# Kernel optimization log

Hardware: AMD Instinct MI355X
Metric: run time of the kernel (lower is better)

Reference implementation:

```python
import jax, jax.numpy as jnp
import numpy as np

N, E, IN, H, L, NB, G = 50000, 300000, 64, 256, 4, 181, 64
EPS = 1e-5
NEG_SLOPE = 0.2


def segment_softmax(e, seg, n):
    m = jax.ops.segment_max(e, seg, num_segments=n)
    a = jnp.exp(e - m[seg])
    d = jax.ops.segment_sum(a, seg, num_segments=n)
    return a / d[seg]


def setup_inputs() -> dict:
    key = jax.random.key(0)
    ks = jax.random.split(key, 32)
    p = lambda k, shape, fan: (jax.random.normal(k, shape, jnp.float32) / np.sqrt(fan)).astype(jnp.float32)
    inp = {}
    inp["x"] = jax.random.normal(ks[0], (N, IN), jnp.float32)
    inp["edge_index"] = jax.random.randint(ks[1], (2, E), 0, N, jnp.int64)
    inp["batch"] = jnp.sort(jax.random.randint(ks[2], (N,), 0, G, jnp.int64))
    inp["W_in"] = p(ks[3], (H, IN), IN); inp["b_in"] = jnp.zeros((H,), jnp.float32)
    inp["Wl"] = p(ks[4], (L, H, H), H); inp["bl"] = jnp.zeros((L, H), jnp.float32)
    inp["Wr"] = p(ks[5], (L, H, H), H); inp["br"] = jnp.zeros((L, H), jnp.float32)
    inp["att"] = p(ks[6], (L, H), H)
    inp["bias_c"] = jnp.zeros((L, H), jnp.float32)
    inp["ln_g"] = jnp.ones((L, H), jnp.float32); inp["ln_b"] = jnp.zeros((L, H), jnp.float32)
    inp["Wg1"] = p(ks[7], (H, H), H); inp["bg1"] = jnp.zeros((H,), jnp.float32)
    inp["Wg2"] = p(ks[8], (1, H), H); inp["bg2"] = jnp.zeros((1,), jnp.float32)
    inp["Ws"] = p(ks[9], (H, H), H); inp["bs"] = jnp.zeros((H,), jnp.float32)
    inp["Wc"] = p(ks[10], (NB, H), H); inp["bc"] = jnp.zeros((NB,), jnp.float32)
    inp["Wr1"] = p(ks[11], (128, H), H); inp["br1"] = jnp.zeros((128,), jnp.float32)
    inp["Wr2"] = p(ks[12], (1, 128), 128); inp["br2"] = jnp.zeros((1,), jnp.float32)
    return inp


def reference(x, edge_index, batch, W_in, b_in, Wl, bl, Wr, br, att, bias_c, ln_g, ln_b,
              Wg1, bg1, Wg2, bg2, Ws, bs, Wc, bc, Wr1, br1, Wr2, br2):
    n = x.shape[0]
    x = x @ W_in.T + b_in  # input projection -> [N,H]
    loops = jnp.arange(n)
    src = jnp.concatenate([edge_index[0], loops])  # GATv2 add_self_loops=True
    dst = jnp.concatenate([edge_index[1], loops])
    for l in range(L):
        x_res = x
        xl = x @ Wl[l].T + bl[l]  # lin_l (source)
        xr = x @ Wr[l].T + br[l]  # lin_r (target)
        h = jax.nn.leaky_relu(xl[src] + xr[dst], NEG_SLOPE)  # [E+N, H]
        e = h @ att[l]                                       # [E+N]
        alpha = segment_softmax(e, dst, n)
        out = jax.ops.segment_sum(alpha[:, None] * xl[src], dst, num_segments=n) + bias_c[l]
        mu = out.mean(-1, keepdims=True)
        var = out.var(-1, keepdims=True)
        out = (out - mu) / jnp.sqrt(var + EPS) * ln_g[l] + ln_b[l]
        x = jax.nn.relu(out) + x_res  # dropout is identity at eval
    gate = jax.nn.relu(x @ Wg1.T + bg1) @ Wg2.T + bg2  # [N,1]
    a = segment_softmax(gate[:, 0], batch, G)
    pooled = jax.ops.segment_sum(a[:, None] * x, batch, num_segments=G)  # [G,H]
    z = jax.nn.relu(pooled @ Ws.T + bs)
    cls_logits = z @ Wc.T + bc                                   # [G,NB]
    residual = jnp.tanh(jax.nn.relu(z @ Wr1.T + br1) @ Wr2.T + br2)[:, 0]  # [G]
    return cls_logits, residual
```

## Files before the change

### kernel.cpp

```cpp
#include <hip/hip_runtime.h>
#include <math.h>

#define N_NODES 50000
#define N_EDGES 300000
#define IN_DIM 64
#define H 256
#define LAYERS 4
#define NB 181
#define NGRAPH 64
#define EE (N_EDGES + N_NODES)
#define NEG_SLOPE 0.2f
#define LN_EPS 1e-5f

typedef unsigned short u16;
typedef __attribute__((ext_vector_type(8))) short short8;
typedef __attribute__((ext_vector_type(4))) float floatx4;

__device__ __forceinline__ u16 f2b(float f) {
  unsigned int u = __builtin_bit_cast(unsigned int, f);
  unsigned int r = (u + 0x7FFFu + ((u >> 16) & 1u)) >> 16;
  return (u16)r;
}
__device__ __forceinline__ float b2f(u16 b) {
  return __builtin_bit_cast(float, ((unsigned int)b) << 16);
}

__device__ __forceinline__ float wave_reduce_sum(float v) {
  #pragma unroll
  for (int off = 32; off > 0; off >>= 1) v += __shfl_xor(v, off, 64);
  return v;
}

__global__ void cast_bf16_kernel(const float* __restrict__ in, u16* __restrict__ out, int n4) {
  int i = blockIdx.x * 256 + threadIdx.x;
  if (i < n4) {
    float4 f = ((const float4*)in)[i];
    ushort4 o;
    o.x = f2b(f.x); o.y = f2b(f.y); o.z = f2b(f.z); o.w = f2b(f.w);
    ((ushort4*)out)[i] = o;
  }
}

__global__ void cast_weights_kernel(
    const float* __restrict__ W_in, const float* __restrict__ Wg1,
    const float* __restrict__ Wl, const float* __restrict__ Wr,
    u16* __restrict__ win_bf, u16* __restrict__ wg1_bf,
    u16* __restrict__ wl_bf, u16* __restrict__ wr_bf)
{
  int i = blockIdx.x * 256 + threadIdx.x;
  int which = blockIdx.y;
  const float* s; u16* dd; int n4;
  if (which == 0)      { s = W_in; dd = win_bf; n4 = H * IN_DIM / 4; }
  else if (which == 1) { s = Wg1;  dd = wg1_bf; n4 = H * H / 4; }
  else if (which == 2) { s = Wl;   dd = wl_bf;  n4 = LAYERS * H * H / 4; }
  else                 { s = Wr;   dd = wr_bf;  n4 = LAYERS * H * H / 4; }
  if (i < n4) {
    float4 f = ((const float4*)s)[i];
    ushort4 o;
    o.x = f2b(f.x); o.y = f2b(f.y); o.z = f2b(f.z); o.w = f2b(f.w);
    ((ushort4*)dd)[i] = o;
  }
}

__global__ void init_counts_kernel(int* __restrict__ cnt) {
  int i = blockIdx.x * 256 + threadIdx.x;
  if (i < N_NODES) cnt[i] = 1;
}

__global__ void count_edges_kernel(const int* __restrict__ dst, int* __restrict__ cnt) {
  int e = blockIdx.x * 256 + threadIdx.x;
  if (e < N_EDGES) atomicAdd(&cnt[dst[e]], 1);
}

__global__ void scan_blocks_kernel(const int* __restrict__ cnt, int* __restrict__ partial,
                                   int* __restrict__ bsums, int n) {
  __shared__ int buf[256];
  int tid = threadIdx.x;
  int i = blockIdx.x * 256 + tid;
  buf[tid] = (i < n) ? cnt[i] : 0;
  __syncthreads();
  #pragma unroll
  for (int off = 1; off < 256; off <<= 1) {
    int t = (tid >= off) ? buf[tid - off] : 0;
    __syncthreads();
    buf[tid] += t;
    __syncthreads();
  }
  if (i < n) partial[i] = buf[tid];
  if (tid == 255) bsums[blockIdx.x] = buf[255];
}

__global__ void scan_sums_kernel(int* __restrict__ bsums, int nblk) {
  __shared__ int buf[256];
  int tid = threadIdx.x;
  buf[tid] = (tid < nblk) ? bsums[tid] : 0;
  __syncthreads();
  #pragma unroll
  for (int off = 1; off < 256; off <<= 1) {
    int t = (tid >= off) ? buf[tid - off] : 0;
    __syncthreads();
    buf[tid] += t;
    __syncthreads();
  }
  if (tid < nblk) bsums[tid] = buf[tid];
}

__global__ void scan_write_kernel(const int* __restrict__ partial, const int* __restrict__ bsums,
                                  int* __restrict__ rowp, int n) {
  int i = blockIdx.x * 256 + threadIdx.x;
  if (i < n) {
    int b = blockIdx.x;
    int off = (b > 0) ? bsums[b - 1] : 0;
    rowp[i + 1] = partial[i] + off;
    if (i == 0) rowp[0] = 0;
  }
}

__global__ void fill_self_kernel(const int* __restrict__ rowp, int* __restrict__ col,
                                 int* __restrict__ fillpos) {
  int i = blockIdx.x * 256 + threadIdx.x;
  if (i < N_NODES) {
    int p = rowp[i];
    col[p] = i;
    fillpos[i] = p + 1;
  }
}

__global__ void fill_edges_kernel(const int* __restrict__ src, const int* __restrict__ dst,
                                  int* __restrict__ fillpos, int* __restrict__ col) {
  int e = blockIdx.x * 256 + threadIdx.x;
  if (e < N_EDGES) {
    int d = dst[e];
    int p = atomicAdd(&fillpos[d], 1);
    col[p] = src[e];
  }
}

#define GTM 128
#define GTK 64
#define LDB 72
#define SSTR 132

__global__ __launch_bounds__(256) void gemm_proj_kernel(
    const u16* __restrict__ A, const u16* __restrict__ W,
    const float* __restrict__ bias, u16* __restrict__ outbf, int M, int K)
{
  __shared__ u16 smem[2 * GTM * LDB];
  u16* As = smem;
  u16* Bs = smem + GTM * LDB;
  int tid = threadIdx.x;
  int lane = tid & 63;
  int wave = tid >> 6;
  int wm = (wave >> 1) * 64;
  int wn = (wave & 1) * 64;
  int bm = blockIdx.y * GTM;
  int n0 = blockIdx.x * 128;
  int lr = tid >> 3;
  int lc = (tid & 7) * 8;

  floatx4 zero4 = {0.f, 0.f, 0.f, 0.f};
  floatx4 acc[4][4];
  #pragma unroll
  for (int i = 0; i < 4; i++)
    #pragma unroll
    for (int j = 0; j < 4; j++) acc[i][j] = zero4;

  int q8 = (lane >> 4) * 8;
  int mrow = lane & 15;

  for (int k0 = 0; k0 < K; k0 += GTK) {
    __syncthreads();
    #pragma unroll
    for (int p = 0; p < 4; p++) {
      int row = lr + p * 32;
      int gr = bm + row;
      short8 av = {0, 0, 0, 0, 0, 0, 0, 0};
      if (gr < M) av = *(const short8*)&A[(size_t)gr * K + k0 + lc];
      *(short8*)&As[row * LDB + lc] = av;
      short8 bv = *(const short8*)&W[(size_t)(n0 + row) * K + k0 + lc];
      *(short8*)&Bs[row * LDB + lc] = bv;
    }
    __syncthreads();
    #pragma unroll
    for (int h = 0; h < 2; h++) {
      short8 af[4], bf[4];
      #pragma unroll
      for (int i = 0; i < 4; i++)
        af[i] = *(const short8*)&As[(wm + i * 16 + mrow) * LDB + h * 32 + q8];
      #pragma unroll
      for (int j = 0; j < 4; j++)
        bf[j] = *(const short8*)&Bs[(wn + j * 16 + mrow) * LDB + h * 32 + q8];
      #pragma unroll
      for (int i = 0; i < 4; i++)
        #pragma unroll
        for (int j = 0; j < 4; j++)
          acc[i][j] = __builtin_amdgcn_mfma_f32_16x16x32_bf16(af[i], bf[j], acc[i][j], 0, 0, 0);
    }
  }

  __syncthreads();
  u16* stage = smem;
  int ccol = lane & 15;
  int crow4 = (lane >> 4) * 4;
  #pragma unroll
  for (int j = 0; j < 4; j++) {
    float bv = bias[n0 + wn + j * 16 + ccol];
    #pragma unroll
    for (int i = 0; i < 4; i++) {
      #pragma unroll
      for (int r = 0; r < 4; r++) {
        int row = wm + i * 16 + crow4 + r;
        stage[row * SSTR + wn + j * 16 + ccol] = f2b(acc[i][j][r] + bv);
      }
    }
  }
  __syncthreads();
  int rr = tid >> 1;
  int c0 = (tid & 1) * 64;
  int grow = bm + rr;
  if (grow < M) {
    const ushort4* sp = (const ushort4*)&stage[rr * SSTR + c0];
    ushort4* gp = (ushort4*)&outbf[(size_t)grow * H + n0 + c0];
    #pragma unroll
    for (int q = 0; q < 16; q++) gp[q] = sp[q];
  }
}

#define DTM 64
#define AST 264
#define SSTR2 132

__global__ __launch_bounds__(256) void gemm_dual2_kernel(
    const u16* __restrict__ A, const u16* __restrict__ Wlb, const u16* __restrict__ Wrb,
    const float* __restrict__ biasL, const float* __restrict__ biasR,
    u16* __restrict__ outL, u16* __restrict__ outR, int M)
{
  __shared__ u16 As[DTM * AST];
  __shared__ u16 Bs[128 * LDB];
  int tid = threadIdx.x;
  int lane = tid & 63;
  int wave = tid >> 6;
  int wn = wave * 32;
  int bm = blockIdx.x * DTM;
  int mrow = lane & 15;
  int q8 = (lane >> 4) * 8;
  int ccol = lane & 15;
  int crow4 = (lane >> 4) * 4;

  {
    int col = (tid & 31) * 8;
    int r0 = tid >> 5;
    #pragma unroll
    for (int it = 0; it < 8; it++) {
      int row = r0 + it * 8;
      int gr = bm + row;
      short8 av = {0, 0, 0, 0, 0, 0, 0, 0};
      if (gr < M) av = *(const short8*)&A[(size_t)gr * H + col];
      *(short8*)&As[row * AST + col] = av;
    }
  }

  floatx4 zero4 = {0.f, 0.f, 0.f, 0.f};

  for (int nt = 0; nt < 4; nt++) {
    const u16* W = (nt < 2) ? Wlb : Wrb;
    const float* bias = (nt < 2) ? biasL : biasR;
    u16* outp = (nt < 2) ? outL : outR;
    int n0 = (nt & 1) * 128;

    floatx4 acc[4][2];
    #pragma unroll
    for (int i = 0; i < 4; i++) {
      acc[i][0] = zero4;
      acc[i][1] = zero4;
    }

    for (int k0 = 0; k0 < H; k0 += 64) {
      __syncthreads();
      {
        int col = (tid & 7) * 8;
        int r0 = tid >> 3;
        #pragma unroll
        for (int p2 = 0; p2 < 4; p2++) {
          int row = r0 + p2 * 32;
          short8 bv = *(const short8*)&W[(size_t)(n0 + row) * H + k0 + col];
          *(short8*)&Bs[row * LDB + col] = bv;
        }
      }
      __syncthreads();
      #pragma unroll
      for (int h = 0; h < 2; h++) {
        short8 af[4], bf[2];
        #pragma unroll
        for (int i = 0; i < 4; i++)
          af[i] = *(const short8*)&As[(i * 16 + mrow) * AST + k0 + h * 32 + q8];
        #pragma unroll
        for (int j = 0; j < 2; j++)
          bf[j] = *(const short8*)&Bs[(wn + j * 16 + mrow) * LDB + h * 32 + q8];
        #pragma unroll
        for (int i = 0; i < 4; i++)
          #pragma unroll
          for (int j = 0; j < 2; j++)
            acc[i][j] = __builtin_amdgcn_mfma_f32_16x16x32_bf16(af[i], bf[j], acc[i][j], 0, 0, 0);
      }
    }

    __syncthreads();
    u16* stage = Bs;
    #pragma unroll
    for (int j = 0; j < 2; j++) {
      float bv = bias[n0 + wn + j * 16 + ccol];
      #pragma unroll
      for (int i = 0; i < 4; i++) {
        #pragma unroll
        for (int r = 0; r < 4; r++) {
          int row = i * 16 + crow4 + r;
          stage[row * SSTR2 + wn + j * 16 + ccol] = f2b(acc[i][j][r] + bv);
        }
      }
    }
    __syncthreads();
    {
      int row = tid >> 2;
      int c0 = (tid & 3) * 32;
      int grow = bm + row;
      if (grow < M) {
        #pragma unroll
        for (int q = 0; q < 8; q++)
          *(ushort4*)&outp[(size_t)grow * H + n0 + c0 + q * 4] =
              *(const ushort4*)&stage[row * SSTR2 + c0 + q * 4];
      }
    }
  }
}

__global__ __launch_bounds__(256) void gemm_gate_kernel(
    const u16* __restrict__ A, const u16* __restrict__ W,
    const float* __restrict__ bias, const float* __restrict__ Wg2,
    float* __restrict__ gate, int M)
{
  __shared__ u16 smem[2 * GTM * LDB];
  u16* As = smem;
  u16* Bs = smem + GTM * LDB;
  int tid = threadIdx.x;
  int lane = tid & 63;
  int wave = tid >> 6;
  int wm = (wave >> 1) * 64;
  int wn = (wave & 1) * 64;
  int bm = blockIdx.y * GTM;
  int bn = blockIdx.x * 128;
  int lr = tid >> 3;
  int lc = (tid & 7) * 8;

  floatx4 zero4 = {0.f, 0.f, 0.f, 0.f};
  floatx4 acc[4][4];
  #pragma unroll
  for (int i = 0; i < 4; i++)
    #pragma unroll
    for (int j = 0; j < 4; j++) acc[i][j] = zero4;

  int q8 = (lane >> 4) * 8;
  int mrow = lane & 15;

  for (int k0 = 0; k0 < H; k0 += GTK) {
    __syncthreads();
    #pragma unroll
    for (int p = 0; p < 4; p++) {
      int row = lr + p * 32;
      int gr = bm + row;
      short8 av = {0, 0, 0, 0, 0, 0, 0, 0};
      if (gr < M) av = *(const short8*)&A[(size_t)gr * H + k0 + lc];
      *(short8*)&As[row * LDB + lc] = av;
      short8 bv = *(const short8*)&W[(size_t)(bn + row) * H + k0 + lc];
      *(short8*)&Bs[row * LDB + lc] = bv;
    }
    __syncthreads();
    #pragma unroll
    for (int h = 0; h < 2; h++) {
      short8 af[4], bf[4];
      #pragma unroll
      for (int i = 0; i < 4; i++)
        af[i] = *(const short8*)&As[(wm + i * 16 + mrow) * LDB + h * 32 + q8];
      #pragma unroll
      for (int j = 0; j < 4; j++)
        bf[j] = *(const short8*)&Bs[(wn + j * 16 + mrow) * LDB + h * 32 + q8];
      #pragma unroll
      for (int i = 0; i < 4; i++)
        #pragma unroll
        for (int j = 0; j < 4; j++)
          acc[i][j] = __builtin_amdgcn_mfma_f32_16x16x32_bf16(af[i], bf[j], acc[i][j], 0, 0, 0);
    }
  }

  int ccol = lane & 15;
  float bv[4], wv[4];
  #pragma unroll
  for (int j = 0; j < 4; j++) {
    int col = bn + wn + j * 16 + ccol;
    bv[j] = bias[col];
    wv[j] = Wg2[col];
  }
  #pragma unroll
  for (int i = 0; i < 4; i++) {
    #pragma unroll
    for (int r = 0; r < 4; r++) {
      float p = 0.f;
      #pragma unroll
      for (int j = 0; j < 4; j++) {
        float hcol = fmaxf(acc[i][j][r] + bv[j], 0.f);
        p += hcol * wv[j];
      }
      p += __shfl_xor(p, 1, 64);
      p += __shfl_xor(p, 2, 64);
      p += __shfl_xor(p, 4, 64);
      p += __shfl_xor(p, 8, 64);
      int row = bm + wm + i * 16 + (lane >> 4) * 4 + r;
      if ((lane & 15) == 0 && row < M) atomicAdd(&gate[row], p);
    }
  }
}

__global__ __launch_bounds__(256) void layer_fused_kernel(
    const u16* __restrict__ xl, const u16* __restrict__ xr,
    u16* __restrict__ xbf,
    const int* __restrict__ rowp, const int* __restrict__ col,
    const float* __restrict__ att, const float* __restrict__ bias_c,
    const float* __restrict__ ln_g, const float* __restrict__ ln_b)
{
  int lane = threadIdx.x & 63;
  int v = blockIdx.x * 4 + (threadIdx.x >> 6);
  if (v >= N_NODES) return;
  int f4 = lane << 2;
  size_t rowbase = (size_t)v * H;
  ushort4 xr4 = *(const ushort4*)&xr[rowbase + f4];
  float xrx = b2f(xr4.x), xry = b2f(xr4.y), xrz = b2f(xr4.z), xrw = b2f(xr4.w);
  float4 attv = *(const float4*)&att[f4];
  int beg = rowp[v], end = rowp[v + 1];
  float m = -INFINITY, d = 0.f;
  float ox = 0.f, oy = 0.f, oz = 0.f, ow = 0.f;
  int p = beg;
  for (; p + 2 <= end; p += 2) {
    int u0 = col[p];
    int u1 = col[p + 1];
    ushort4 a04 = *(const ushort4*)&xl[(size_t)u0 * H + f4];
    ushort4 a14 = *(const ushort4*)&xl[(size_t)u1 * H + f4];
    float a0x = b2f(a04.x), a0y = b2f(a04.y), a0z = b2f(a04.z), a0w = b2f(a04.w);
    float a1x = b2f(a14.x), a1y = b2f(a14.y), a1z = b2f(a14.z), a1w = b2f(a14.w);
    float t0x = a0x + xrx; t0x = t0x > 0.f ? t0x : NEG_SLOPE * t0x;
    float t0y = a0y + xry; t0y = t0y > 0.f ? t0y : NEG_SLOPE * t0y;
    float t0z = a0z + xrz; t0z = t0z > 0.f ? t0z : NEG_SLOPE * t0z;
    float t0w = a0w + xrw; t0w = t0w > 0.f ? t0w : NEG_SLOPE * t0w;
    float t1x = a1x + xrx; t1x = t1x > 0.f ? t1x : NEG_SLOPE * t1x;
    float t1y = a1y + xry; t1y = t1y > 0.f ? t1y : NEG_SLOPE * t1y;
    float t1z = a1z + xrz; t1z = t1z > 0.f ? t1z : NEG_SLOPE * t1z;
    float t1w = a1w + xrw; t1w = t1w > 0.f ? t1w : NEG_SLOPE * t1w;
    float pe0 = t0x * attv.x + t0y * attv.y + t0z * attv.z + t0w * attv.w;
    float pe1 = t1x * attv.x + t1y * attv.y + t1z * attv.z + t1w * attv.w;
    #pragma unroll
    for (int off = 32; off > 0; off >>= 1) {
      pe0 += __shfl_xor(pe0, off, 64);
      pe1 += __shfl_xor(pe1, off, 64);
    }
    float mn = fmaxf(m, fmaxf(pe0, pe1));
    float sc = __expf(m - mn);
    float w0 = __expf(pe0 - mn);
    float w1 = __expf(pe1 - mn);
    d = fmaf(d, sc, w0 + w1);
    ox = fmaf(ox, sc, fmaf(w0, a0x, w1 * a1x));
    oy = fmaf(oy, sc, fmaf(w0, a0y, w1 * a1y));
    oz = fmaf(oz, sc, fmaf(w0, a0z, w1 * a1z));
    ow = fmaf(ow, sc, fmaf(w0, a0w, w1 * a1w));
    m = mn;
  }
  if (p < end) {
    int u0 = col[p];
    ushort4 a04 = *(const ushort4*)&xl[(size_t)u0 * H + f4];
    float a0x = b2f(a04.x), a0y = b2f(a04.y), a0z = b2f(a04.z), a0w = b2f(a04.w);
    float t0x = a0x + xrx; t0x = t0x > 0.f ? t0x : NEG_SLOPE * t0x;
    float t0y = a0y + xry; t0y = t0y > 0.f ? t0y : NEG_SLOPE * t0y;
    float t0z = a0z + xrz; t0z = t0z > 0.f ? t0z : NEG_SLOPE * t0z;
    float t0w = a0w + xrw; t0w = t0w > 0.f ? t0w : NEG_SLOPE * t0w;
    float pe0 = t0x * attv.x + t0y * attv.y + t0z * attv.z + t0w * attv.w;
    pe0 = wave_reduce_sum(pe0);
    float mn = fmaxf(m, pe0);
    float sc = __expf(m - mn);
    float w0 = __expf(pe0 - mn);
    d = fmaf(d, sc, w0);
    ox = fmaf(ox, sc, w0 * a0x);
    oy = fmaf(oy, sc, w0 * a0y);
    oz = fmaf(oz, sc, w0 * a0z);
    ow = fmaf(ow, sc, w0 * a0w);
    m = mn;
  }
  float invd = 1.0f / d;
  float4 bc4 = *(const float4*)&bias_c[f4];
  ox = ox * invd + bc4.x;
  oy = oy * invd + bc4.y;
  oz = oz * invd + bc4.z;
  ow = ow * invd + bc4.w;
  float s = wave_reduce_sum(ox + oy + oz + ow);
  float mean = s * (1.0f / H);
  float cx = ox - mean, cy = oy - mean, cz = oz - mean, cw = ow - mean;
  float sq = wave_reduce_sum(cx * cx + cy * cy + cz * cz + cw * cw);
  float rstd = rsqrtf(sq * (1.0f / H) + LN_EPS);
  float4 g4 = *(const float4*)&ln_g[f4];
  float4 b4 = *(const float4*)&ln_b[f4];
  ushort4 xres4 = *(const ushort4*)&xbf[rowbase + f4];
  float yx = fmaxf(cx * rstd * g4.x + b4.x, 0.f) + b2f(xres4.x);
  float yy = fmaxf(cy * rstd * g4.y + b4.y, 0.f) + b2f(xres4.y);
  float yz = fmaxf(cz * rstd * g4.z + b4.z, 0.f) + b2f(xres4.z);
  float yw = fmaxf(cw * rstd * g4.w + b4.w, 0.f) + b2f(xres4.w);
  ushort4 yb;
  yb.x = f2b(yx); yb.y = f2b(yy); yb.z = f2b(yz); yb.w = f2b(yw);
  *(ushort4*)&xbf[rowbase + f4] = yb;
}

__global__ void gate_init_kernel(float* __restrict__ gate, const float* __restrict__ bg2,
                                 int* __restrict__ gstart, int* __restrict__ gend) {
  int i = blockIdx.x * 256 + threadIdx.x;
  if (i < N_NODES) gate[i] = bg2[0];
  if (i < NGRAPH) { gstart[i] = 0; gend[i] = 0; }
}

__global__ void gbounds_kernel(const int* __restrict__ batch, int* __restrict__ gstart,
                               int* __restrict__ gend) {
  int i = blockIdx.x * 256 + threadIdx.x;
  if (i < N_NODES) {
    int b = batch[i];
    if (i == 0 || batch[i - 1] != b) gstart[b] = i;
    if (i == N_NODES - 1 || batch[i + 1] != b) gend[b] = i + 1;
  }
}

__global__ __launch_bounds__(256) void pool_prep_kernel(
    const float* __restrict__ gate, const int* __restrict__ gstart,
    const int* __restrict__ gend, float* __restrict__ gmax, float* __restrict__ gdinv,
    float* __restrict__ pooled)
{
  __shared__ float red[256];
  int g = blockIdx.x, tid = threadIdx.x;
  pooled[(size_t)g * H + tid] = 0.f;
  int s = gstart[g], e = gend[g];
  float lm = -INFINITY;
  for (int i = s + tid; i < e; i += 256) lm = fmaxf(lm, gate[i]);
  red[tid] = lm;
  __syncthreads();
  for (int off = 128; off; off >>= 1) {
    if (tid < off) red[tid] = fmaxf(red[tid], red[tid + off]);
    __syncthreads();
  }
  float m = red[0];
  __syncthreads();
  float lsum = 0.0f;
  for (int i = s + tid; i < e; i += 256) lsum += __expf(gate[i] - m);
  red[tid] = lsum;
  __syncthreads();
  for (int off = 128; off; off >>= 1) {
    if (tid < off) red[tid] += red[tid + off];
    __syncthreads();
  }
  if (tid == 0) {
    gmax[g] = m;
    gdinv[g] = (s < e) ? 1.0f / red[0] : 0.0f;
  }
}

__global__ __launch_bounds__(256) void pool_accum_kernel(
    const float* __restrict__ gate, const u16* __restrict__ xbf,
    const int* __restrict__ batch, const float* __restrict__ gmax,
    const float* __restrict__ gdinv, float* __restrict__ pooled)
{
  __shared__ float wl[128];
  __shared__ int gl[128];
  int b0 = blockIdx.x * 128;
  int tid = threadIdx.x;
  if (tid < 128) {
    int v = b0 + tid;
    if (v < N_NODES) {
      int g = batch[v];
      gl[tid] = g;
      wl[tid] = __expf(gate[v] - gmax[g]) * gdinv[g];
    } else {
      gl[tid] = -1;
      wl[tid] = 0.f;
    }
  }
  __syncthreads();
  int cnt = min(128, N_NODES - b0);
  float acc = 0.f;
  int cur = gl[0];
  for (int j = 0; j < cnt; j++) {
    int g = gl[j];
    if (g != cur) {
      atomicAdd(&pooled[(size_t)cur * H + tid], acc);
      acc = 0.f;
      cur = g;
    }
    acc += wl[j] * b2f(xbf[(size_t)(b0 + j) * H + tid]);
  }
  if (cur >= 0) atomicAdd(&pooled[(size_t)cur * H + tid], acc);
}

__global__ __launch_bounds__(256) void head_kernel(
    const float* __restrict__ pooled,
    const float* __restrict__ Ws, const float* __restrict__ bs,
    const float* __restrict__ Wc, const float* __restrict__ bc,
    const float* __restrict__ Wr1, const float* __restrict__ br1,
    const float* __restrict__ Wr2, const float* __restrict__ br2,
    float* __restrict__ out)
{
  __shared__ float psh[256];
  __shared__ float zsh[256];
  __shared__ float r1sh[128];
  int g = blockIdx.x, tid = threadIdx.x;
  psh[tid] = pooled[(size_t)g * H + tid];
  __syncthreads();
  {
    float acc = bs[tid];
    const float4* wr = (const float4*)&Ws[(size_t)tid * H];
    for (int k4 = 0; k4 < H / 4; k4++) {
      float4 wv = wr[k4];
      float4 av = *(const float4*)&psh[k4 * 4];
      acc += av.x * wv.x + av.y * wv.y + av.z * wv.z + av.w * wv.w;
    }
    zsh[tid] = fmaxf(acc, 0.f);
  }
  __syncthreads();
  if (tid < NB) {
    float acc = bc[tid];
    const float4* wr = (const float4*)&Wc[(size_t)tid * H];
    for (int k4 = 0; k4 < H / 4; k4++) {
      float4 wv = wr[k4];
      float4 av = *(const float4*)&zsh[k4 * 4];
      acc += av.x * wv.x + av.y * wv.y + av.z * wv.z + av.w * wv.w;
    }
    out[(size_t)g * NB + tid] = acc;
  }
  if (tid < 128) {
    float acc = br1[tid];
    const float4* wr = (const float4*)&Wr1[(size_t)tid * H];
    for (int k4 = 0; k4 < H / 4; k4++) {
      float4 wv = wr[k4];
      float4 av = *(const float4*)&zsh[k4 * 4];
      acc += av.x * wv.x + av.y * wv.y + av.z * wv.z + av.w * wv.w;
    }
    r1sh[tid] = fmaxf(acc, 0.f);
  }
  __syncthreads();
  if (tid < 64) {
    float s2 = r1sh[tid] * Wr2[tid] + r1sh[tid + 64] * Wr2[tid + 64];
    s2 = wave_reduce_sum(s2);
    if (tid == 0) out[(size_t)NGRAPH * NB + g] = tanhf(s2 + br2[0]);
  }
}

extern "C" void kernel_launch(void* const* d_in, const int* in_sizes, int n_in,
                              void* d_out, int out_size, void* d_ws, size_t ws_size,
                              hipStream_t stream) {
  const float* x_in   = (const float*)d_in[0];
  const int*   eidx   = (const int*)d_in[1];
  const int*   batch  = (const int*)d_in[2];
  const float* W_in   = (const float*)d_in[3];
  const float* b_in   = (const float*)d_in[4];
  const float* Wl     = (const float*)d_in[5];
  const float* bl     = (const float*)d_in[6];
  const float* Wr     = (const float*)d_in[7];
  const float* br     = (const float*)d_in[8];
  const float* att    = (const float*)d_in[9];
  const float* bias_c = (const float*)d_in[10];
  const float* ln_g   = (const float*)d_in[11];
  const float* ln_b   = (const float*)d_in[12];
  const float* Wg1    = (const float*)d_in[13];
  const float* bg1    = (const float*)d_in[14];
  const float* Wg2    = (const float*)d_in[15];
  const float* bg2    = (const float*)d_in[16];
  const float* Ws     = (const float*)d_in[17];
  const float* bs     = (const float*)d_in[18];
  const float* Wc     = (const float*)d_in[19];
  const float* bc     = (const float*)d_in[20];
  const float* Wr1    = (const float*)d_in[21];
  const float* br1    = (const float*)d_in[22];
  const float* Wr2    = (const float*)d_in[23];
  const float* br2    = (const float*)d_in[24];
  float* out = (float*)d_out;

  char* w = (char*)d_ws;
  u16* x_bf   = (u16*)w;    w += sizeof(u16) * (size_t)N_NODES * H;
  u16* xl_bf  = (u16*)w;    w += sizeof(u16) * (size_t)N_NODES * H;
  u16* xr_bf  = (u16*)w;    w += sizeof(u16) * (size_t)N_NODES * H;
  u16* xin_bf = (u16*)w;    w += sizeof(u16) * (size_t)N_NODES * IN_DIM;
  u16* win_bf = (u16*)w;    w += sizeof(u16) * (size_t)H * IN_DIM;
  u16* wl_bf  = (u16*)w;    w += sizeof(u16) * (size_t)LAYERS * H * H;
  u16* wr_bf  = (u16*)w;    w += sizeof(u16) * (size_t)LAYERS * H * H;
  u16* wg1_bf = (u16*)w;    w += sizeof(u16) * (size_t)H * H;
  float* pooled = (float*)w; w += sizeof(float) * NGRAPH * H;
  float* gate = (float*)w;  w += sizeof(float) * N_NODES;
  float* gmax = (float*)w;  w += sizeof(float) * NGRAPH;
  float* gdinv= (float*)w;  w += sizeof(float) * NGRAPH;
  int* cnt    = (int*)w;    w += sizeof(int) * N_NODES;
  int* rowp   = (int*)w;    w += sizeof(int) * (N_NODES + 1);
  int* col    = (int*)w;    w += sizeof(int) * EE;
  int* partial= (int*)w;    w += sizeof(int) * N_NODES;
  int* bsums  = (int*)w;    w += sizeof(int) * 256;
  int* gstart = (int*)w;    w += sizeof(int) * NGRAPH;
  int* gend   = (int*)w;    w += sizeof(int) * NGRAPH;
  (void)ws_size; (void)n_in; (void)in_sizes; (void)out_size;

  const int* src = eidx;
  const int* dst = eidx + N_EDGES;
  int nblkN = (N_NODES + 255) / 256;
  int nblkE = (N_EDGES + 255) / 256;
  int mtiles = (N_NODES + GTM - 1) / GTM;
  int mtiles2 = (N_NODES + DTM - 1) / DTM;

  init_counts_kernel<<<nblkN, 256, 0, stream>>>(cnt);
  count_edges_kernel<<<nblkE, 256, 0, stream>>>(dst, cnt);
  scan_blocks_kernel<<<nblkN, 256, 0, stream>>>(cnt, partial, bsums, N_NODES);
  scan_sums_kernel<<<1, 256, 0, stream>>>(bsums, nblkN);
  scan_write_kernel<<<nblkN, 256, 0, stream>>>(partial, bsums, rowp, N_NODES);
  fill_self_kernel<<<nblkN, 256, 0, stream>>>(rowp, col, cnt);
  fill_edges_kernel<<<nblkE, 256, 0, stream>>>(src, dst, cnt, col);

  {
    int maxn4 = LAYERS * H * H / 4;
    dim3 gcast((maxn4 + 255) / 256, 4);
    cast_weights_kernel<<<gcast, 256, 0, stream>>>(W_in, Wg1, Wl, Wr,
                                                   win_bf, wg1_bf, wl_bf, wr_bf);
    int n4 = N_NODES * IN_DIM / 4;
    cast_bf16_kernel<<<(n4 + 255) / 256, 256, 0, stream>>>(x_in, xin_bf, n4);
  }

  dim3 gproj(2, mtiles);
  gemm_proj_kernel<<<gproj, 256, 0, stream>>>(xin_bf, win_bf, b_in, x_bf, N_NODES, IN_DIM);

  int nblkV = N_NODES / 4;
  for (int l = 0; l < LAYERS; l++) {
    gemm_dual2_kernel<<<mtiles2, 256, 0, stream>>>(x_bf,
        wl_bf + (size_t)l * H * H, wr_bf + (size_t)l * H * H,
        bl + l * H, br + l * H, xl_bf, xr_bf, N_NODES);
    layer_fused_kernel<<<nblkV, 256, 0, stream>>>(xl_bf, xr_bf, x_bf, rowp, col,
        att + l * H, bias_c + l * H, ln_g + l * H, ln_b + l * H);
  }

  gate_init_kernel<<<nblkN, 256, 0, stream>>>(gate, bg2, gstart, gend);
  dim3 ggate(2, mtiles);
  gemm_gate_kernel<<<ggate, 256, 0, stream>>>(x_bf, wg1_bf, bg1, Wg2, gate, N_NODES);

  gbounds_kernel<<<nblkN, 256, 0, stream>>>(batch, gstart, gend);
  pool_prep_kernel<<<NGRAPH, 256, 0, stream>>>(gate, gstart, gend, gmax, gdinv, pooled);
  pool_accum_kernel<<<(N_NODES + 127) / 128, 256, 0, stream>>>(gate, x_bf, batch, gmax, gdinv, pooled);

  head_kernel<<<NGRAPH, 256, 0, stream>>>(pooled, Ws, bs, Wc, bc, Wr1, br1, Wr2, br2, out);
}
```

Measured before the change: 639.7 us.

## Switch activations to fp16 and gather two edges per wave with packed half math

All stored activations and weights move from bf16 to fp16, and the GEMMs use the f16 MFMA. The GAT aggregation kernel is restructured so each half-wave processes a different edge with 16-byte loads of 8 features per lane. The leaky-relu and attention dot product run on packed half2 math with fdot2, and the two half-wave partial softmax states are merged at the end. This is meant to halve the reduction shuffle depth per edge and cut ALU work in the gather-bound layer kernel, at the cost of fp16 range and precision risk on activations and attention logits.

```diff
diff --git a/kernel.cpp b/kernel.cpp
--- a/kernel.cpp
+++ b/kernel.cpp
@@ -13,16 +13,16 @@
 #define LN_EPS 1e-5f
 
 typedef unsigned short u16;
-typedef __attribute__((ext_vector_type(8))) short short8;
+typedef __attribute__((ext_vector_type(8))) _Float16 half8;
+typedef __attribute__((ext_vector_type(2))) _Float16 half2v;
 typedef __attribute__((ext_vector_type(4))) float floatx4;
 
-__device__ __forceinline__ u16 f2b(float f) {
-  unsigned int u = __builtin_bit_cast(unsigned int, f);
-  unsigned int r = (u + 0x7FFFu + ((u >> 16) & 1u)) >> 16;
-  return (u16)r;
-}
-__device__ __forceinline__ float b2f(u16 b) {
-  return __builtin_bit_cast(float, ((unsigned int)b) << 16);
+__device__ __forceinline__ u16 f2h(float f) {
+  _Float16 h = (_Float16)f;
+  return __builtin_bit_cast(u16, h);
+}
+__device__ __forceinline__ float h2f(u16 b) {
+  return (float)__builtin_bit_cast(_Float16, b);
 }
 
 __device__ __forceinline__ float wave_reduce_sum(float v) {
@@ -31,12 +31,12 @@
   return v;
 }
 
-__global__ void cast_bf16_kernel(const float* __restrict__ in, u16* __restrict__ out, int n4) {
+__global__ void cast_f16_kernel(const float* __restrict__ in, u16* __restrict__ out, int n4) {
   int i = blockIdx.x * 256 + threadIdx.x;
   if (i < n4) {
     float4 f = ((const float4*)in)[i];
     ushort4 o;
-    o.x = f2b(f.x); o.y = f2b(f.y); o.z = f2b(f.z); o.w = f2b(f.w);
+    o.x = f2h(f.x); o.y = f2h(f.y); o.z = f2h(f.z); o.w = f2h(f.w);
     ((ushort4*)out)[i] = o;
   }
 }
@@ -44,20 +44,20 @@
 __global__ void cast_weights_kernel(
     const float* __restrict__ W_in, const float* __restrict__ Wg1,
     const float* __restrict__ Wl, const float* __restrict__ Wr,
-    u16* __restrict__ win_bf, u16* __restrict__ wg1_bf,
-    u16* __restrict__ wl_bf, u16* __restrict__ wr_bf)
+    u16* __restrict__ win_h, u16* __restrict__ wg1_h,
+    u16* __restrict__ wl_h, u16* __restrict__ wr_h)
 {
   int i = blockIdx.x * 256 + threadIdx.x;
   int which = blockIdx.y;
   const float* s; u16* dd; int n4;
-  if (which == 0)      { s = W_in; dd = win_bf; n4 = H * IN_DIM / 4; }
-  else if (which == 1) { s = Wg1;  dd = wg1_bf; n4 = H * H / 4; }
-  else if (which == 2) { s = Wl;   dd = wl_bf;  n4 = LAYERS * H * H / 4; }
-  else                 { s = Wr;   dd = wr_bf;  n4 = LAYERS * H * H / 4; }
+  if (which == 0)      { s = W_in; dd = win_h; n4 = H * IN_DIM / 4; }
+  else if (which == 1) { s = Wg1;  dd = wg1_h; n4 = H * H / 4; }
+  else if (which == 2) { s = Wl;   dd = wl_h;  n4 = LAYERS * H * H / 4; }
+  else                 { s = Wr;   dd = wr_h;  n4 = LAYERS * H * H / 4; }
   if (i < n4) {
     float4 f = ((const float4*)s)[i];
     ushort4 o;
-    o.x = f2b(f.x); o.y = f2b(f.y); o.z = f2b(f.z); o.w = f2b(f.w);
+    o.x = f2h(f.x); o.y = f2h(f.y); o.z = f2h(f.z); o.w = f2h(f.w);
     ((ushort4*)dd)[i] = o;
   }
 }
@@ -143,7 +143,7 @@
 
 __global__ __launch_bounds__(256) void gemm_proj_kernel(
     const u16* __restrict__ A, const u16* __restrict__ W,
-    const float* __restrict__ bias, u16* __restrict__ outbf, int M, int K)
+    const float* __restrict__ bias, u16* __restrict__ outh, int M, int K)
 {
   __shared__ u16 smem[2 * GTM * LDB];
   u16* As = smem;
@@ -174,27 +174,27 @@
     for (int p = 0; p < 4; p++) {
       int row = lr + p * 32;
       int gr = bm + row;
-      short8 av = {0, 0, 0, 0, 0, 0, 0, 0};
-      if (gr < M) av = *(const short8*)&A[(size_t)gr * K + k0 + lc];
-      *(short8*)&As[row * LDB + lc] = av;
-      short8 bv = *(const short8*)&W[(size_t)(n0 + row) * K + k0 + lc];
-      *(short8*)&Bs[row * LDB + lc] = bv;
+      uint4 av = {0, 0, 0, 0};
+      if (gr < M) av = *(const uint4*)&A[(size_t)gr * K + k0 + lc];
+      *(uint4*)&As[row * LDB + lc] = av;
+      uint4 bv = *(const uint4*)&W[(size_t)(n0 + row) * K + k0 + lc];
+      *(uint4*)&Bs[row * LDB + lc] = bv;
     }
     __syncthreads();
     #pragma unroll
     for (int h = 0; h < 2; h++) {
-      short8 af[4], bf[4];
+      half8 af[4], bf[4];
       #pragma unroll
       for (int i = 0; i < 4; i++)
-        af[i] = *(const short8*)&As[(wm + i * 16 + mrow) * LDB + h * 32 + q8];
+        af[i] = *(const half8*)&As[(wm + i * 16 + mrow) * LDB + h * 32 + q8];
       #pragma unroll
       for (int j = 0; j < 4; j++)
-        bf[j] = *(const short8*)&Bs[(wn + j * 16 + mrow) * LDB + h * 32 + q8];
+        bf[j] = *(const half8*)&Bs[(wn + j * 16 + mrow) * LDB + h * 32 + q8];
       #pragma unroll
       for (int i = 0; i < 4; i++)
         #pragma unroll
         for (int j = 0; j < 4; j++)
-          acc[i][j] = __builtin_amdgcn_mfma_f32_16x16x32_bf16(af[i], bf[j], acc[i][j], 0, 0, 0);
+          acc[i][j] = __builtin_amdgcn_mfma_f32_16x16x32_f16(af[i], bf[j], acc[i][j], 0, 0, 0);
     }
   }
 
@@ -210,7 +210,7 @@
       #pragma unroll
       for (int r = 0; r < 4; r++) {
         int row = wm + i * 16 + crow4 + r;
-        stage[row * SSTR + wn + j * 16 + ccol] = f2b(acc[i][j][r] + bv);
+        stage[row * SSTR + wn + j * 16 + ccol] = f2h(acc[i][j][r] + bv);
       }
     }
   }
@@ -220,7 +220,7 @@
   int grow = bm + rr;
   if (grow < M) {
     const ushort4* sp = (const ushort4*)&stage[rr * SSTR + c0];
-    ushort4* gp = (ushort4*)&outbf[(size_t)grow * H + n0 + c0];
+    ushort4* gp = (ushort4*)&outh[(size_t)grow * H + n0 + c0];
     #pragma unroll
     for (int q = 0; q < 16; q++) gp[q] = sp[q];
   }
@@ -254,9 +254,9 @@
     for (int it = 0; it < 8; it++) {
       int row = r0 + it * 8;
       int gr = bm + row;
-      short8 av = {0, 0, 0, 0, 0, 0, 0, 0};
-      if (gr < M) av = *(const short8*)&A[(size_t)gr * H + col];
-      *(short8*)&As[row * AST + col] = av;
+      uint4 av = {0, 0, 0, 0};
+      if (gr < M) av = *(const uint4*)&A[(size_t)gr * H + col];
+      *(uint4*)&As[row * AST + col] = av;
     }
   }
 
@@ -283,25 +283,25 @@
         #pragma unroll
         for (int p2 = 0; p2 < 4; p2++) {
           int row = r0 + p2 * 32;
-          short8 bv = *(const short8*)&W[(size_t)(n0 + row) * H + k0 + col];
-          *(short8*)&Bs[row * LDB + col] = bv;
+          uint4 bv = *(const uint4*)&W[(size_t)(n0 + row) * H + k0 + col];
+          *(uint4*)&Bs[row * LDB + col] = bv;
         }
       }
       __syncthreads();
       #pragma unroll
       for (int h = 0; h < 2; h++) {
-        short8 af[4], bf[2];
+        half8 af[4], bf[2];
         #pragma unroll
         for (int i = 0; i < 4; i++)
-          af[i] = *(const short8*)&As[(i * 16 + mrow) * AST + k0 + h * 32 + q8];
+          af[i] = *(const half8*)&As[(i * 16 + mrow) * AST + k0 + h * 32 + q8];
         #pragma unroll
         for (int j = 0; j < 2; j++)
-          bf[j] = *(const short8*)&Bs[(wn + j * 16 + mrow) * LDB + h * 32 + q8];
+          bf[j] = *(const half8*)&Bs[(wn + j * 16 + mrow) * LDB + h * 32 + q8];
         #pragma unroll
         for (int i = 0; i < 4; i++)
           #pragma unroll
           for (int j = 0; j < 2; j++)
-            acc[i][j] = __builtin_amdgcn_mfma_f32_16x16x32_bf16(af[i], bf[j], acc[i][j], 0, 0, 0);
+            acc[i][j] = __builtin_amdgcn_mfma_f32_16x16x32_f16(af[i], bf[j], acc[i][j], 0, 0, 0);
       }
     }
 
@@ -315,7 +315,7 @@
         #pragma unroll
         for (int r = 0; r < 4; r++) {
           int row = i * 16 + crow4 + r;
-          stage[row * SSTR2 + wn + j * 16 + ccol] = f2b(acc[i][j][r] + bv);
+          stage[row * SSTR2 + wn + j * 16 + ccol] = f2h(acc[i][j][r] + bv);
         }
       }
     }
@@ -368,27 +368,27 @@
     for (int p = 0; p < 4; p++) {
       int row = lr + p * 32;
       int gr = bm + row;
-      short8 av = {0, 0, 0, 0, 0, 0, 0, 0};
-      if (gr < M) av = *(const short8*)&A[(size_t)gr * H + k0 + lc];
-      *(short8*)&As[row * LDB + lc] = av;
-      short8 bv = *(const short8*)&W[(size_t)(bn + row) * H + k0 + lc];
-      *(short8*)&Bs[row * LDB + lc] = bv;
+      uint4 av = {0, 0, 0, 0};
+      if (gr < M) av = *(const uint4*)&A[(size_t)gr * H + k0 + lc];
+      *(uint4*)&As[row * LDB + lc] = av;
+      uint4 bv = *(const uint4*)&W[(size_t)(bn + row) * H + k0 + lc];
+      *(uint4*)&Bs[row * LDB + lc] = bv;
     }
     __syncthreads();
     #pragma unroll
     for (int h = 0; h < 2; h++) {
-      short8 af[4], bf[4];
+      half8 af[4], bf[4];
       #pragma unroll
       for (int i = 0; i < 4; i++)
-        af[i] = *(const short8*)&As[(wm + i * 16 + mrow) * LDB + h * 32 + q8];
+        af[i] = *(const half8*)&As[(wm + i * 16 + mrow) * LDB + h * 32 + q8];
       #pragma unroll
       for (int j = 0; j < 4; j++)
-        bf[j] = *(const short8*)&Bs[(wn + j * 16 + mrow) * LDB + h * 32 + q8];
+        bf[j] = *(const half8*)&Bs[(wn + j * 16 + mrow) * LDB + h * 32 + q8];
       #pragma unroll
       for (int i = 0; i < 4; i++)
         #pragma unroll
         for (int j = 0; j < 4; j++)
-          acc[i][j] = __builtin_amdgcn_mfma_f32_16x16x32_bf16(af[i], bf[j], acc[i][j], 0, 0, 0);
+          acc[i][j] = __builtin_amdgcn_mfma_f32_16x16x32_f16(af[i], bf[j], acc[i][j], 0, 0, 0);
     }
   }
 
@@ -422,7 +422,7 @@
 
 __global__ __launch_bounds__(256) void layer_fused_kernel(
     const u16* __restrict__ xl, const u16* __restrict__ xr,
-    u16* __restrict__ xbf,
+    u16* __restrict__ xst,
     const int* __restrict__ rowp, const int* __restrict__ col,
     const float* __restrict__ att, const float* __restrict__ bias_c,
     const float* __restrict__ ln_g, const float* __restrict__ ln_b)
@@ -430,89 +430,110 @@
   int lane = threadIdx.x & 63;
   int v = blockIdx.x * 4 + (threadIdx.x >> 6);
   if (v >= N_NODES) return;
-  int f4 = lane << 2;
+  int slot = lane >> 5;
+  int fl = lane & 31;
+  int f8 = fl << 3;
   size_t rowbase = (size_t)v * H;
-  ushort4 xr4 = *(const ushort4*)&xr[rowbase + f4];
-  float xrx = b2f(xr4.x), xry = b2f(xr4.y), xrz = b2f(xr4.z), xrw = b2f(xr4.w);
-  float4 attv = *(const float4*)&att[f4];
+
+  uint4 xrq = *(const uint4*)&xr[rowbase + f8];
+  half2v xrh[4] = {
+    __builtin_bit_cast(half2v, xrq.x), __builtin_bit_cast(half2v, xrq.y),
+    __builtin_bit_cast(half2v, xrq.z), __builtin_bit_cast(half2v, xrq.w)};
+  float4 attA = *(const float4*)&att[f8];
+  float4 attB = *(const float4*)&att[f8 + 4];
+  half2v ath[4] = {
+    {(_Float16)attA.x, (_Float16)attA.y}, {(_Float16)attA.z, (_Float16)attA.w},
+    {(_Float16)attB.x, (_Float16)attB.y}, {(_Float16)attB.z, (_Float16)attB.w}};
+  const half2v kslope = {(_Float16)NEG_SLOPE, (_Float16)NEG_SLOPE};
+
   int beg = rowp[v], end = rowp[v + 1];
   float m = -INFINITY, d = 0.f;
-  float ox = 0.f, oy = 0.f, oz = 0.f, ow = 0.f;
-  int p = beg;
-  for (; p + 2 <= end; p += 2) {
+  float o[8] = {0.f, 0.f, 0.f, 0.f, 0.f, 0.f, 0.f, 0.f};
+
+  for (int p = beg; p < end; p += 2) {
+    int valid1 = (p + 1 < end);
     int u0 = col[p];
-    int u1 = col[p + 1];
-    ushort4 a04 = *(const ushort4*)&xl[(size_t)u0 * H + f4];
-    ushort4 a14 = *(const ushort4*)&xl[(size_t)u1 * H + f4];
-    float a0x = b2f(a04.x), a0y = b2f(a04.y), a0z = b2f(a04.z), a0w = b2f(a04.w);
-    float a1x = b2f(a14.x), a1y = b2f(a14.y), a1z = b2f(a14.z), a1w = b2f(a14.w);
-    float t0x = a0x + xrx; t0x = t0x > 0.f ? t0x : NEG_SLOPE * t0x;
-    float t0y = a0y + xry; t0y = t0y > 0.f ? t0y : NEG_SLOPE * t0y;
-    float t0z = a0z + xrz; t0z = t0z > 0.f ? t0z : NEG_SLOPE * t0z;
-    float t0w = a0w + xrw; t0w = t0w > 0.f ? t0w : NEG_SLOPE * t0w;
-    float t1x = a1x + xrx; t1x = t1x > 0.f ? t1x : NEG_SLOPE * t1x;
-    float t1y = a1y + xry; t1y = t1y > 0.f ? t1y : NEG_SLOPE * t1y;
-    float t1z = a1z + xrz; t1z = t1z > 0.f ? t1z : NEG_SLOPE * t1z;
-    float t1w = a1w + xrw; t1w = t1w > 0.f ? t1w : NEG_SLOPE * t1w;
-    float pe0 = t0x * attv.x + t0y * attv.y + t0z * attv.z + t0w * attv.w;
-    float pe1 = t1x * attv.x + t1y * attv.y + t1z * attv.z + t1w * attv.w;
-    #pragma unroll
-    for (int off = 32; off > 0; off >>= 1) {
-      pe0 += __shfl_xor(pe0, off, 64);
-      pe1 += __shfl_xor(pe1, off, 64);
-    }
-    float mn = fmaxf(m, fmaxf(pe0, pe1));
+    int u1 = valid1 ? col[p + 1] : u0;
+    int u = slot ? u1 : u0;
+    uint4 aq = *(const uint4*)&xl[(size_t)u * H + f8];
+    half2v ah[4] = {
+      __builtin_bit_cast(half2v, aq.x), __builtin_bit_cast(half2v, aq.y),
+      __builtin_bit_cast(half2v, aq.z), __builtin_bit_cast(half2v, aq.w)};
+    float pe = 0.f;
+    #pragma unroll
+    for (int q = 0; q < 4; q++) {
+      half2v h = ah[q] + xrh[q];
+      half2v l = __builtin_elementwise_max(h, h * kslope);
+#if __has_builtin(__builtin_amdgcn_fdot2)
+      pe = __builtin_amdgcn_fdot2(l, ath[q], pe, false);
+#else
+      pe += (float)l[0] * (float)ath[q][0] + (float)l[1] * (float)ath[q][1];
+#endif
+    }
+    #pragma unroll
+    for (int off = 16; off > 0; off >>= 1) pe += __shfl_xor(pe, off, 64);
+    if (slot && !valid1) pe = -INFINITY;
+    float peO = __shfl_xor(pe, 32, 64);
+    float mn = fmaxf(m, fmaxf(pe, peO));
     float sc = __expf(m - mn);
-    float w0 = __expf(pe0 - mn);
-    float w1 = __expf(pe1 - mn);
-    d = fmaf(d, sc, w0 + w1);
-    ox = fmaf(ox, sc, fmaf(w0, a0x, w1 * a1x));
-    oy = fmaf(oy, sc, fmaf(w0, a0y, w1 * a1y));
-    oz = fmaf(oz, sc, fmaf(w0, a0z, w1 * a1z));
-    ow = fmaf(ow, sc, fmaf(w0, a0w, w1 * a1w));
+    float w = __expf(pe - mn);
+    d = fmaf(d, sc, w);
+    #pragma unroll
+    for (int q = 0; q < 8; q++) {
+      float af = (float)((q & 1) ? ah[q >> 1][1] : ah[q >> 1][0]);
+      o[q] = fmaf(o[q], sc, w * af);
+    }
     m = mn;
   }
-  if (p < end) {
-    int u0 = col[p];
-    ushort4 a04 = *(const ushort4*)&xl[(size_t)u0 * H + f4];
-    float a0x = b2f(a04.x), a0y = b2f(a04.y), a0z = b2f(a04.z), a0w = b2f(a04.w);
-    float t0x = a0x + xrx; t0x = t0x > 0.f ? t0x : NEG_SLOPE * t0x;
-    float t0y = a0y + xry; t0y = t0y > 0.f ? t0y : NEG_SLOPE * t0y;
-    float t0z = a0z + xrz; t0z = t0z > 0.f ? t0z : NEG_SLOPE * t0z;
-    float t0w = a0w + xrw; t0w = t0w > 0.f ? t0w : NEG_SLOPE * t0w;
-    float pe0 = t0x * attv.x + t0y * attv.y + t0z * attv.z + t0w * attv.w;
-    pe0 = wave_reduce_sum(pe0);
-    float mn = fmaxf(m, pe0);
-    float sc = __expf(m - mn);
-    float w0 = __expf(pe0 - mn);
-    d = fmaf(d, sc, w0);
-    ox = fmaf(ox, sc, w0 * a0x);
-    oy = fmaf(oy, sc, w0 * a0y);
-    oz = fmaf(oz, sc, w0 * a0z);
-    ow = fmaf(ow, sc, w0 * a0w);
-    m = mn;
-  }
+
+  d += __shfl_xor(d, 32, 64);
+  #pragma unroll
+  for (int q = 0; q < 8; q++) o[q] += __shfl_xor(o[q], 32, 64);
+
   float invd = 1.0f / d;
-  float4 bc4 = *(const float4*)&bias_c[f4];
-  ox = ox * invd + bc4.x;
-  oy = oy * invd + bc4.y;
-  oz = oz * invd + bc4.z;
-  ow = ow * invd + bc4.w;
-  float s = wave_reduce_sum(ox + oy + oz + ow);
-  float mean = s * (1.0f / H);
-  float cx = ox - mean, cy = oy - mean, cz = oz - mean, cw = ow - mean;
-  float sq = wave_reduce_sum(cx * cx + cy * cy + cz * cz + cw * cw);
+  float4 bcA = *(const float4*)&bias_c[f8];
+  float4 bcB = *(const float4*)&bias_c[f8 + 4];
+  float bc[8] = {bcA.x, bcA.y, bcA.z, bcA.w, bcB.x, bcB.y, bcB.z, bcB.w};
+  float ox[8];
+  float part = 0.f;
+  #pragma unroll
+  for (int q = 0; q < 8; q++) {
+    ox[q] = fmaf(o[q], invd, bc[q]);
+    part += ox[q];
+  }
+  #pragma unroll
+  for (int off = 16; off > 0; off >>= 1) part += __shfl_xor(part, off, 64);
+  float mean = part * (1.0f / H);
+  float sq = 0.f;
+  #pragma unroll
+  for (int q = 0; q < 8; q++) {
+    ox[q] -= mean;
+    sq = fmaf(ox[q], ox[q], sq);
+  }
+  #pragma unroll
+  for (int off = 16; off > 0; off >>= 1) sq += __shfl_xor(sq, off, 64);
   float rstd = rsqrtf(sq * (1.0f / H) + LN_EPS);
-  float4 g4 = *(const float4*)&ln_g[f4];
-  float4 b4 = *(const float4*)&ln_b[f4];
-  ushort4 xres4 = *(const ushort4*)&xbf[rowbase + f4];
-  float yx = fmaxf(cx * rstd * g4.x + b4.x, 0.f) + b2f(xres4.x);
-  float yy = fmaxf(cy * rstd * g4.y + b4.y, 0.f) + b2f(xres4.y);
-  float yz = fmaxf(cz * rstd * g4.z + b4.z, 0.f) + b2f(xres4.z);
-  float yw = fmaxf(cw * rstd * g4.w + b4.w, 0.f) + b2f(xres4.w);
-  ushort4 yb;
-  yb.x = f2b(yx); yb.y = f2b(yy); yb.z = f2b(yz); yb.w = f2b(yw);
-  *(ushort4*)&xbf[rowbase + f4] = yb;
+
+  if (slot == 0) {
+    float4 gA = *(const float4*)&ln_g[f8];
+    float4 gB = *(const float4*)&ln_g[f8 + 4];
+    float4 bA = *(const float4*)&ln_b[f8];
+    float4 bB = *(const float4*)&ln_b[f8 + 4];
+    float gg[8] = {gA.x, gA.y, gA.z, gA.w, gB.x, gB.y, gB.z, gB.w};
+    float bb[8] = {bA.x, bA.y, bA.z, bA.w, bB.x, bB.y, bB.z, bB.w};
+    uint4 resq = *(const uint4*)&xst[rowbase + f8];
+    half2v rh[4] = {
+      __builtin_bit_cast(half2v, resq.x), __builtin_bit_cast(half2v, resq.y),
+      __builtin_bit_cast(half2v, resq.z), __builtin_bit_cast(half2v, resq.w)};
+    u16 yout[8];
+    #pragma unroll
+    for (int q = 0; q < 8; q++) {
+      float res = (float)((q & 1) ? rh[q >> 1][1] : rh[q >> 1][0]);
+      float y = fmaxf(fmaf(ox[q] * rstd, gg[q], bb[q]), 0.f) + res;
+      yout[q] = f2h(y);
+    }
+    *(uint4*)&xst[rowbase + f8] = *(const uint4*)yout;
+  }
 }
 
 __global__ void gate_init_kernel(float* __restrict__ gate, const float* __restrict__ bg2,
@@ -566,7 +587,7 @@
 }
 
 __global__ __launch_bounds__(256) void pool_accum_kernel(
-    const float* __restrict__ gate, const u16* __restrict__ xbf,
+    const float* __restrict__ gate, const u16* __restrict__ xh,
     const int* __restrict__ batch, const float* __restrict__ gmax,
     const float* __restrict__ gdinv, float* __restrict__ pooled)
 {
@@ -596,7 +617,7 @@
       acc = 0.f;
       cur = g;
     }
-    acc += wl[j] * b2f(xbf[(size_t)(b0 + j) * H + tid]);
+    acc += wl[j] * h2f(xh[(size_t)(b0 + j) * H + tid]);
   }
   if (cur >= 0) atomicAdd(&pooled[(size_t)cur * H + tid], acc);
 }
@@ -685,14 +706,14 @@
   float* out = (float*)d_out;
 
   char* w = (char*)d_ws;
-  u16* x_bf   = (u16*)w;    w += sizeof(u16) * (size_t)N_NODES * H;
-  u16* xl_bf  = (u16*)w;    w += sizeof(u16) * (size_t)N_NODES * H;
-  u16* xr_bf  = (u16*)w;    w += sizeof(u16) * (size_t)N_NODES * H;
-  u16* xin_bf = (u16*)w;    w += sizeof(u16) * (size_t)N_NODES * IN_DIM;
-  u16* win_bf = (u16*)w;    w += sizeof(u16) * (size_t)H * IN_DIM;
-  u16* wl_bf  = (u16*)w;    w += sizeof(u16) * (size_t)LAYERS * H * H;
-  u16* wr_bf  = (u16*)w;    w += sizeof(u16) * (size_t)LAYERS * H * H;
-  u16* wg1_bf = (u16*)w;    w += sizeof(u16) * (size_t)H * H;
+  u16* x_h    = (u16*)w;    w += sizeof(u16) * (size_t)N_NODES * H;
+  u16* xl_h   = (u16*)w;    w += sizeof(u16) * (size_t)N_NODES * H;
+  u16* xr_h   = (u16*)w;    w += sizeof(u16) * (size_t)N_NODES * H;
+  u16* xin_h  = (u16*)w;    w += sizeof(u16) * (size_t)N_NODES * IN_DIM;
+  u16* win_h  = (u16*)w;    w += sizeof(u16) * (size_t)H * IN_DIM;
+  u16* wl_h   = (u16*)w;    w += sizeof(u16) * (size_t)LAYERS * H * H;
+  u16* wr_h   = (u16*)w;    w += sizeof(u16) * (size_t)LAYERS * H * H;
+  u16* wg1_h  = (u16*)w;    w += sizeof(u16) * (size_t)H * H;
   float* pooled = (float*)w; w += sizeof(float) * NGRAPH * H;
   float* gate = (float*)w;  w += sizeof(float) * N_NODES;
   float* gmax = (float*)w;  w += sizeof(float) * NGRAPH;
@@ -725,30 +746,30 @@
     int maxn4 = LAYERS * H * H / 4;
     dim3 gcast((maxn4 + 255) / 256, 4);
     cast_weights_kernel<<<gcast, 256, 0, stream>>>(W_in, Wg1, Wl, Wr,
-                                                   win_bf, wg1_bf, wl_bf, wr_bf);
+                                                   win_h, wg1_h, wl_h, wr_h);
     int n4 = N_NODES * IN_DIM / 4;
-    cast_bf16_kernel<<<(n4 + 255) / 256, 256, 0, stream>>>(x_in, xin_bf, n4);
+    cast_f16_kernel<<<(n4 + 255) / 256, 256, 0, stream>>>(x_in, xin_h, n4);
   }
 
   dim3 gproj(2, mtiles);
-  gemm_proj_kernel<<<gproj, 256, 0, stream>>>(xin_bf, win_bf, b_in, x_bf, N_NODES, IN_DIM);
+  gemm_proj_kernel<<<gproj, 256, 0, stream>>>(xin_h, win_h, b_in, x_h, N_NODES, IN_DIM);
 
   int nblkV = N_NODES / 4;
   for (int l = 0; l < LAYERS; l++) {
-    gemm_dual2_kernel<<<mtiles2, 256, 0, stream>>>(x_bf,
-        wl_bf + (size_t)l * H * H, wr_bf + (size_t)l * H * H,
-        bl + l * H, br + l * H, xl_bf, xr_bf, N_NODES);
-    layer_fused_kernel<<<nblkV, 256, 0, stream>>>(xl_bf, xr_bf, x_bf, rowp, col,
+    gemm_dual2_kernel<<<mtiles2, 256, 0, stream>>>(x_h,
+        wl_h + (size_t)l * H * H, wr_h + (size_t)l * H * H,
+        bl + l * H, br + l * H, xl_h, xr_h, N_NODES);
+    layer_fused_kernel<<<nblkV, 256, 0, stream>>>(xl_h, xr_h, x_h, rowp, col,
         att + l * H, bias_c + l * H, ln_g + l * H, ln_b + l * H);
   }
 
   gate_init_kernel<<<nblkN, 256, 0, stream>>>(gate, bg2, gstart, gend);
   dim3 ggate(2, mtiles);
-  gemm_gate_kernel<<<ggate, 256, 0, stream>>>(x_bf, wg1_bf, bg1, Wg2, gate, N_NODES);
+  gemm_gate_kernel<<<ggate, 256, 0, stream>>>(x_h, wg1_h, bg1, Wg2, gate, N_NODES);
 
   gbounds_kernel<<<nblkN, 256, 0, stream>>>(batch, gstart, gend);
   pool_prep_kernel<<<NGRAPH, 256, 0, stream>>>(gate, gstart, gend, gmax, gdinv, pooled);
-  pool_accum_kernel<<<(N_NODES + 127) / 128, 256, 0, stream>>>(gate, x_bf, batch, gmax, gdinv, pooled);
+  pool_accum_kernel<<<(N_NODES + 127) / 128, 256, 0, stream>>>(gate, x_h, batch, gmax, gdinv, pooled);
 
   head_kernel<<<NGRAPH, 256, 0, stream>>>(pooled, Ws, bs, Wc, bc, Wr1, br1, Wr2, br2, out);
 }
```

New measurement: 653.3 us. +2.1%, slower.
